# Kernel tuning notes

Measured on AMD Instinct MI355X. Metric: run time of the kernel, lower is better.

The kernel has to match this reference:

```python
import jax, jax.numpy as jnp
import numpy as np
from functools import partial

B, S, V, H, NH, NKV, M, L = 2, 2048, 51200, 1536, 24, 4, 8960, 8
DH = H // NH  # 64
EPS = 1e-6


def setup_inputs() -> dict:
    key = jax.random.key(0)
    ks = jax.random.split(key, 16)
    sc = 0.02
    w = lambda k, shape: jax.random.normal(k, shape, jnp.float32) * sc
    inp = {
        "input_ids": jax.random.randint(ks[0], (B, S), 0, V),
        "attention_mask": jnp.ones((B, S), jnp.float32),
        "embed": w(ks[1], (V, H)),
        "Wq": w(ks[2], (L, H, H)),          "bq": jnp.zeros((L, H), jnp.float32),
        "Wk": w(ks[3], (L, H, NKV * DH)),   "bk": jnp.zeros((L, NKV * DH), jnp.float32),
        "Wv": w(ks[4], (L, H, NKV * DH)),   "bv": jnp.zeros((L, NKV * DH), jnp.float32),
        "Wo": w(ks[5], (L, H, H)),
        "ln1": jnp.ones((L, H), jnp.float32),
        "ln2": jnp.ones((L, H), jnp.float32),
        "Wg": w(ks[6], (L, H, M)),
        "Wu": w(ks[7], (L, H, M)),
        "Wd": w(ks[8], (L, M, H)),
        "norm_w": jnp.ones((H,), jnp.float32),
        "W1": w(ks[9], (H, H)), "b1": jnp.zeros((H,), jnp.float32),
        "W2": w(ks[10], (H, 1)), "b2": jnp.zeros((1,), jnp.float32),
    }
    inv_freq = 1.0 / (10000.0 ** (jnp.arange(0, DH, 2, dtype=jnp.float32) / DH))
    freqs = jnp.outer(jnp.arange(S, dtype=jnp.float32), inv_freq)  # [S, DH/2]
    emb = jnp.concatenate([freqs, freqs], axis=-1)                 # [S, DH]
    inp["cos"] = jnp.cos(emb)
    inp["sin"] = jnp.sin(emb)
    return inp


def _rms(x, w):
    var = jnp.mean(x.astype(jnp.float32) ** 2, axis=-1, keepdims=True)
    return w * (x * jax.lax.rsqrt(var + EPS)).astype(x.dtype)


def _rotate_half(x):
    x1, x2 = jnp.split(x, 2, axis=-1)
    return jnp.concatenate([-x2, x1], axis=-1)


def _forward(input_ids, attention_mask, embed, Wq, bq, Wk, bk, Wv, bv, Wo,
             ln1, ln2, Wg, Wu, Wd, norm_w, W1, b1, W2, b2, cos, sin):
    scale = 1.0 / np.sqrt(DH)
    b, s = input_ids.shape
    c = cos[None, :s, None, :]  # [1,S,1,DH]
    sn = sin[None, :s, None, :]
    rope = lambda t: t * c + _rotate_half(t) * sn
    mask0 = attention_mask[:, None, None, :] == 0  # [B,1,1,S]

    def block(x, p):
        wq, bq_, wk, bk_, wv, bv_, wo, ln1w, ln2w, wg, wu, wd = p
        h = _rms(x, ln1w)
        q = (h @ wq + bq_).reshape(b, s, NH, DH)
        k = (h @ wk + bk_).reshape(b, s, NKV, DH)
        v = (h @ wv + bv_).reshape(b, s, NKV, DH)
        q, k = rope(q), rope(k)
        k = jnp.repeat(k, NH // NKV, axis=2)  # GQA expand to NH heads
        v = jnp.repeat(v, NH // NKV, axis=2)
        scores = jnp.einsum('bqhd,bkhd->bhqk', q, k) * scale
        scores = jnp.where(mask0, -1e10, scores)
        probs = jax.nn.softmax(scores, axis=-1)  # dropout: eval mode (identity)
        attn = jnp.einsum('bhqk,bkhd->bqhd', probs, v).reshape(b, s, H)
        x = x + attn @ wo
        h = _rms(x, ln2w)
        x = x + (jax.nn.sigmoid(h @ wg) * (h @ wu)) @ wd
        return x, None

    x = embed[input_ids]  # [B,S,H]
    x, _ = jax.lax.scan(block, x, (Wq, bq, Wk, bk, Wv, bv, Wo, ln1, ln2, Wg, Wu, Wd))
    x = _rms(x, norm_w)
    h = jax.nn.gelu(x @ W1 + b1, approximate=False)  # torch nn.GELU default = exact
    return h @ W2 + b2  # [B,S,1]


def reference(input_ids, attention_mask, embed, Wq, bq, Wk, bk, Wv, bv, Wo,
              ln1, ln2, Wg, Wu, Wd, norm_w, W1, b1, W2, b2, cos, sin):
    return _forward(input_ids, attention_mask, embed, Wq, bq, Wk, bk, Wv, bv, Wo,
                    ln1, ln2, Wg, Wu, Wd, norm_w, W1, b1, W2, b2, cos, sin)
```

## Files before the change

### kernel.cpp

```cpp
#include <hip/hip_runtime.h>

typedef float f32x4 __attribute__((ext_vector_type(4)));
typedef short s16x8 __attribute__((ext_vector_type(8)));
typedef unsigned short u16;
typedef unsigned short u16x4 __attribute__((ext_vector_type(4)));
typedef unsigned short u16x8 __attribute__((ext_vector_type(8)));
typedef unsigned int u32x2 __attribute__((ext_vector_type(2)));

__device__ __forceinline__ float bf2f(u16 u){ union{unsigned int i; float f;} v; v.i=((unsigned int)u)<<16; return v.f; }
__device__ __forceinline__ u16 f2bf(float f){ union{float f; unsigned int i;} v; v.f=f; return (u16)((v.i + 0x7FFFu + ((v.i>>16)&1u))>>16); }
__device__ __forceinline__ float aexp2(float x){ float r; asm("v_exp_f32 %0, %1" : "=v"(r) : "v"(x)); return r; }
__device__ __forceinline__ unsigned int cvtpk(float lo, float hi){ unsigned int r; asm("v_cvt_pk_bf16_f32 %0, %1, %2" : "=v"(r) : "v"(lo), "v"(hi)); return r; }

#define LOG2E 1.44269504089f

__device__ __forceinline__ void gld16(const void* gp, void* lp){
  __builtin_amdgcn_global_load_lds((__attribute__((address_space(1))) void*)(void*)gp,
                                   (__attribute__((address_space(3))) void*)lp, 16, 0, 0);
}

__global__ __launch_bounds__(256) void k_embed(const int* __restrict__ ids, const float* __restrict__ emb, float* __restrict__ x){
  int r = blockIdx.x;
  int id = ids[r];
  const f32x4* src = (const f32x4*)(emb + (size_t)id*1536);
  f32x4* dst = (f32x4*)(x + (size_t)r*1536);
  for (int i = threadIdx.x; i < 384; i += 256) dst[i] = src[i];
}

__global__ __launch_bounds__(256) void k_rms(const float* __restrict__ x, const float* __restrict__ w, u16* __restrict__ h){
  int r = blockIdx.x, tid = threadIdx.x;
  const f32x4* xr = (const f32x4*)(x + (size_t)r*1536);
  f32x4 v0 = xr[tid];
  float ss = v0.x*v0.x + v0.y*v0.y + v0.z*v0.z + v0.w*v0.w;
  f32x4 v1 = {0,0,0,0};
  if (tid < 128){ v1 = xr[256+tid]; ss += v1.x*v1.x + v1.y*v1.y + v1.z*v1.z + v1.w*v1.w; }
  #pragma unroll
  for (int off=32; off; off>>=1) ss += __shfl_xor(ss, off, 64);
  __shared__ float red[4];
  if ((tid&63)==0) red[tid>>6] = ss;
  __syncthreads();
  float tot = red[0]+red[1]+red[2]+red[3];
  float invr = rsqrtf(tot*(1.f/1536.f) + 1e-6f);
  const f32x4* w4 = (const f32x4*)w;
  u16x4* h4 = (u16x4*)(h + (size_t)r*1536);
  {
    f32x4 wv = w4[tid];
    u16x4 o; o.x=f2bf(v0.x*invr*wv.x); o.y=f2bf(v0.y*invr*wv.y); o.z=f2bf(v0.z*invr*wv.z); o.w=f2bf(v0.w*invr*wv.w);
    h4[tid] = o;
  }
  if (tid < 128){
    f32x4 wv = w4[256+tid];
    u16x4 o; o.x=f2bf(v1.x*invr*wv.x); o.y=f2bf(v1.y*invr*wv.y); o.z=f2bf(v1.z*invr*wv.z); o.w=f2bf(v1.w*invr*wv.w);
    h4[256+tid] = o;
  }
}

__global__ __launch_bounds__(256) void k_rms_add(float* __restrict__ x, const float* __restrict__ P, const float* __restrict__ w, u16* __restrict__ h){
  int r = blockIdx.x, tid = threadIdx.x;
  f32x4* xr = (f32x4*)(x + (size_t)r*1536);
  const f32x4* pr = (const f32x4*)(P + (size_t)r*1536);
  f32x4 v0 = xr[tid], p0 = pr[tid];
  v0.x+=p0.x; v0.y+=p0.y; v0.z+=p0.z; v0.w+=p0.w;
  xr[tid] = v0;
  float ss = v0.x*v0.x + v0.y*v0.y + v0.z*v0.z + v0.w*v0.w;
  f32x4 v1 = {0,0,0,0};
  if (tid < 128){
    v1 = xr[256+tid]; f32x4 p1 = pr[256+tid];
    v1.x+=p1.x; v1.y+=p1.y; v1.z+=p1.z; v1.w+=p1.w;
    xr[256+tid] = v1;
    ss += v1.x*v1.x + v1.y*v1.y + v1.z*v1.z + v1.w*v1.w;
  }
  #pragma unroll
  for (int off=32; off; off>>=1) ss += __shfl_xor(ss, off, 64);
  __shared__ float red[4];
  if ((tid&63)==0) red[tid>>6] = ss;
  __syncthreads();
  float tot = red[0]+red[1]+red[2]+red[3];
  float invr = rsqrtf(tot*(1.f/1536.f) + 1e-6f);
  const f32x4* w4 = (const f32x4*)w;
  u16x4* h4 = (u16x4*)(h + (size_t)r*1536);
  {
    f32x4 wv = w4[tid];
    u16x4 o; o.x=f2bf(v0.x*invr*wv.x); o.y=f2bf(v0.y*invr*wv.y); o.z=f2bf(v0.z*invr*wv.z); o.w=f2bf(v0.w*invr*wv.w);
    h4[tid] = o;
  }
  if (tid < 128){
    f32x4 wv = w4[256+tid];
    u16x4 o; o.x=f2bf(v1.x*invr*wv.x); o.y=f2bf(v1.y*invr*wv.y); o.z=f2bf(v1.z*invr*wv.z); o.w=f2bf(v1.w*invr*wv.w);
    h4[256+tid] = o;
  }
}

__device__ __forceinline__ void cvt_tile(const float* src, int K, int N, u16* dst, int k0, int n0, int roff, int mode){
  __shared__ float T[64*72];
  int tid = threadIdx.x;
  #pragma unroll
  for (int j=0;j<4;++j){
    int i = tid + j*256;
    int row = i>>4, nf = i&15;
    f32x4 vv = *(const f32x4*)(src + (size_t)(k0+row)*N + n0 + nf*4);
    *(f32x4*)&T[row*72 + nf*4] = vv;
  }
  __syncthreads();
  #pragma unroll
  for (int j=0;j<2;++j){
    int i = tid + j*256;
    int n = i>>3, kc = i&7;
    u16x8 o;
    #pragma unroll
    for (int m=0;m<8;++m) o[m] = f2bf(T[(kc*8+m)*72 + n]);
    int gn = n0 + n;
    int dr = (mode==0) ? (roff + gn) : (((gn>>4)<<5) + ((mode==2)?16:0) + (gn&15));
    *(u16x8*)(dst + (size_t)dr*K + k0 + kc*8) = o;
  }
}

__global__ __launch_bounds__(256) void k_cvt_layer(
  const float* __restrict__ Wq, const float* __restrict__ Wk, const float* __restrict__ Wv,
  const float* __restrict__ Wo, const float* __restrict__ Wg, const float* __restrict__ Wu,
  const float* __restrict__ Wd, u16* qkvt, u16* wot, u16* gut, u16* wdt)
{
  const float* src; int K, N; u16* dst; int roff=0, mode=0;
  switch (blockIdx.y){
    case 0: src=Wq; K=1536; N=1536; dst=qkvt; break;
    case 1: src=Wk; K=1536; N=256;  dst=qkvt; roff=1536; break;
    case 2: src=Wv; K=1536; N=256;  dst=qkvt; roff=1792; break;
    case 3: src=Wo; K=1536; N=1536; dst=wot;  break;
    case 4: src=Wg; K=1536; N=8960; dst=gut;  mode=1; break;
    case 5: src=Wu; K=1536; N=8960; dst=gut;  mode=2; break;
    default: src=Wd; K=8960; N=1536; dst=wdt; break;
  }
  int ntn = N>>6;
  int nt = (K>>6)*ntn;
  int t = blockIdx.x;
  if (t >= nt) return;
  cvt_tile(src, K, N, dst, (t/ntn)<<6, (t%ntn)<<6, roff, mode);
}

__global__ __launch_bounds__(256) void k_cvt_one(const float* __restrict__ src, u16* __restrict__ dst){
  int t = blockIdx.x;
  cvt_tile(src, 1536, 1536, dst, (t/24)<<6, (t%24)<<6, 0, 0);
}

#define MODE_QKV 0
#define MODE_WO 1
#define MODE_GATEUP 2
#define MODE_DOWN 3
#define MODE_W1 4

template<int MODE>
__global__ __launch_bounds__(256) void k_gemm(
  const u16* __restrict__ A, const u16* __restrict__ Bt, int K,
  int jobsPerXcd, int nc, int ksplit, int klen,
  const float* __restrict__ bq_, const float* __restrict__ bk_, const float* __restrict__ bv_,
  float* __restrict__ xio, float* __restrict__ Pf,
  const float* __restrict__ cosT, const float* __restrict__ sinT,
  u16* __restrict__ o0, u16* __restrict__ o1, u16* __restrict__ o2)
{
  int bid = blockIdx.x;
  int xcd = bid & 7, j = bid >> 3;
  int job = xcd*jobsPerXcd + (j >> 5);
  if (job >= nc*ksplit) return;
  int rowb = j & 31;
  int col = job / ksplit;
  int ks  = job - col*ksplit;
  int kbase = ks*klen;
  int nt = klen >> 5;

  __shared__ __align__(16) u16 As[4][4096], Bs[4][4096];
  int tid = threadIdx.x;
  int lane = tid & 63, w = tid >> 6;
  int wr = w >> 1, wc = w & 1;
  int row0 = rowb * 128, col0 = col * 128;
  int l15 = lane & 15, l4 = lane >> 4;
  f32x4 acc[4][4] = {};
  const u16* aBase = A + (size_t)row0*K;
  const u16* bBase = Bt + (size_t)col0*K;
  int rr0 = tid & 127, kb0 = tid >> 7;
  int kb1 = kb0 + 2;

  auto stage = [&](int bf, int kt){
    gld16(aBase + (size_t)rr0*K + kt + kb0*8, &As[bf][tid*8]);
    gld16(bBase + (size_t)rr0*K + kt + kb0*8, &Bs[bf][tid*8]);
    gld16(aBase + (size_t)rr0*K + kt + kb1*8, &As[bf][(256+tid)*8]);
    gld16(bBase + (size_t)rr0*K + kt + kb1*8, &Bs[bf][(256+tid)*8]);
  };
  stage(0, kbase); stage(1, kbase+32); stage(2, kbase+64);

  for (int t = 0; t < nt; ++t){
    if (t < nt-2)       asm volatile("s_waitcnt vmcnt(8)" ::: "memory");
    else if (t == nt-2) asm volatile("s_waitcnt vmcnt(4)" ::: "memory");
    else                asm volatile("s_waitcnt vmcnt(0)" ::: "memory");
    __builtin_amdgcn_s_barrier();
    __builtin_amdgcn_sched_barrier(0);
    if (t+3 < nt) stage((t+3)&3, kbase + (t+3)*32);
    const u16* Ab = As[t&3];
    const u16* Bb = Bs[t&3];
    s16x8 af[4], bf_[4];
    #pragma unroll
    for (int i=0;i<4;++i) af[i]  = *(const s16x8*)&Ab[((l4<<7) + wr*64 + i*16 + l15)*8];
    #pragma unroll
    for (int jj=0;jj<4;++jj) bf_[jj] = *(const s16x8*)&Bb[((l4<<7) + wc*64 + jj*16 + l15)*8];
    __builtin_amdgcn_s_setprio(1);
    #pragma unroll
    for (int i=0;i<4;++i)
      #pragma unroll
      for (int jj=0;jj<4;++jj)
        acc[i][jj] = __builtin_amdgcn_mfma_f32_16x16x32_bf16(af[i], bf_[jj], acc[i][jj], 0, 0, 0);
    __builtin_amdgcn_s_setprio(0);
  }

  #pragma unroll
  for (int i=0;i<4;++i)
    #pragma unroll
    for (int jj=0;jj<4;++jj)
      #pragma unroll
      for (int r=0;r<4;++r){
        int row = row0 + wr*64 + i*16 + l4*4 + r;
        int c   = col0 + wc*64 + jj*16 + l15;
        float v = acc[i][jj][r];
        if constexpr (MODE == MODE_QKV){
          int b = row >> 11, s = row & 2047;
          if (c < 1536){
            int d = c & 63, hd = c >> 6;
            float vv = v + bq_[c];
            float pv = acc[i][jj^2][r] + bq_[c^32];
            float cv = cosT[s*64+d], sv = sinT[s*64+d];
            float sgn = (d<32) ? -1.f : 1.f;
            float o = (vv*cv + sgn*pv*sv)*(0.125f*LOG2E);
            o0[(size_t)(b*24+hd)*131072 + (size_t)(s>>6)*4096
               + (s&63)*64 + (((d>>3)^(s&7))<<3) + (d&7)] = f2bf(o);
          } else if (c < 1792){
            int c2 = c - 1536, d = c2 & 63, kv = c2 >> 6;
            float vv = v + bk_[c2];
            float pv = acc[i][jj^2][r] + bk_[c2^32];
            float cv = cosT[s*64+d], sv = sinT[s*64+d];
            float sgn = (d<32) ? -1.f : 1.f;
            float o = vv*cv + sgn*pv*sv;
            o1[(size_t)(b*4+kv)*131072 + (size_t)(s>>6)*4096
               + (s&63)*64 + (((d>>3)^(s&7))<<3) + (d&7)] = f2bf(o);
          } else {
            int c2 = c - 1792, d = c2 & 63, kv = c2 >> 6;
            float vv = v + bv_[c2];
            o2[(size_t)(b*4+kv)*131072 + (size_t)(s>>6)*4096
               + d*64 + ((((s>>3)&7)^(d&7))<<3) + (s&7)] = f2bf(vv);
          }
        } else if constexpr (MODE == MODE_WO){
          xio[(size_t)row*1536 + c] += v;
        } else if constexpr (MODE == MODE_W1){
          v += bq_[c];
          float ge = 0.5f * v * (1.f + erff(v * 0.70710678118f));
          o0[(size_t)row*1536 + c] = f2bf(ge);
        }
      }
}

template<int MODE>
__global__ __launch_bounds__(512,2) void k_gemm256(
  const u16* __restrict__ A, const u16* __restrict__ Bt, int K,
  int nrt, int ksplit, int klen,
  float* __restrict__ xio, float* __restrict__ Pf, u16* __restrict__ o0)
{
  int bid = blockIdx.x;
  int wgid = (bid & 7)*(gridDim.x >> 3) + (bid >> 3);
  int nj = nrt*ksplit;
  int ct = wgid / nj; int r2 = wgid - ct*nj;
  int rt = r2 / ksplit; int ks = r2 - rt*ksplit;

  __shared__ __align__(16) u16 lds[2][2][16384];
  int tid = threadIdx.x;
  int lane = tid & 63, wid = tid >> 6;
  int wm = wid >> 2, wn = wid & 3;
  int l15 = lane & 15, l4 = lane >> 4;
  int lsw = l15 & 7;
  int row0 = rt*256, col0 = ct*256;
  int kbase = ks*klen*64;

  const u16* aB = A  + (size_t)row0*K + kbase;
  const u16* bB = Bt + (size_t)col0*K + kbase;
  int rsub = tid >> 3;
  int gsw  = (lane & 7) ^ ((lane >> 3) & 7);

  f32x4 acc[8][4] = {};

  auto sgA = [&](int bf, int kt, int c){
    gld16(aB + (size_t)(c*64 + rsub)*K + kt*64 + gsw*8, &lds[bf][0][(c*512+tid)*8]);
  };
  auto sgB = [&](int bf, int kt, int c){
    gld16(bB + (size_t)(c*64 + rsub)*K + kt*64 + gsw*8, &lds[bf][1][(c*512+tid)*8]);
  };

  sgB(0,0,0); sgB(0,0,1); sgB(0,0,2); sgB(0,0,3);
  sgA(0,0,0); sgA(0,0,2); sgA(0,0,1); sgA(0,0,3);

  for (int t = 0; t < klen; ++t){
    int b = t & 1, nb = b ^ 1;
    bool hasNext = (t+1 < klen);
    const u16* Ab = lds[b][0];
    const u16* Bb = lds[b][1];

    asm volatile("s_waitcnt vmcnt(2)" ::: "memory");
    __builtin_amdgcn_s_barrier();
    __builtin_amdgcn_sched_barrier(0);
    if (hasNext){ sgB(nb, t+1, 0); sgB(nb, t+1, 1); }

    s16x8 bf_[4][2];
    #pragma unroll
    for (int j=0;j<4;++j)
      #pragma unroll
      for (int ksu=0;ksu<2;++ksu)
        bf_[j][ksu] = *(const s16x8*)&Bb[(wn*64 + j*16 + l15)*64 + (((ksu*4+l4)^lsw)<<3)];

    {
      s16x8 af[2][2];
      #pragma unroll
      for (int ii=0;ii<2;++ii)
        #pragma unroll
        for (int ksu=0;ksu<2;++ksu)
          af[ii][ksu] = *(const s16x8*)&Ab[(wm*128 + ii*16 + l15)*64 + (((ksu*4+l4)^lsw)<<3)];
      __builtin_amdgcn_s_setprio(1);
      #pragma unroll
      for (int ii=0;ii<2;++ii)
        #pragma unroll
        for (int j=0;j<4;++j)
          #pragma unroll
          for (int ksu=0;ksu<2;++ksu)
            acc[ii][j] = __builtin_amdgcn_mfma_f32_16x16x32_bf16(af[ii][ksu], bf_[j][ksu], acc[ii][j], 0,0,0);
      __builtin_amdgcn_s_setprio(0);
    }
    if (hasNext){ sgB(nb, t+1, 2); sgB(nb, t+1, 3); }
    {
      s16x8 af[2][2];
      #pragma unroll
      for (int ii=0;ii<2;++ii)
        #pragma unroll
        for (int ksu=0;ksu<2;++ksu)
          af[ii][ksu] = *(const s16x8*)&Ab[(wm*128 + 32 + ii*16 + l15)*64 + (((ksu*4+l4)^lsw)<<3)];
      __builtin_amdgcn_s_setprio(1);
      #pragma unroll
      for (int ii=0;ii<2;++ii)
        #pragma unroll
        for (int j=0;j<4;++j)
          #pragma unroll
          for (int ksu=0;ksu<2;++ksu)
            acc[2+ii][j] = __builtin_amdgcn_mfma_f32_16x16x32_bf16(af[ii][ksu], bf_[j][ksu], acc[2+ii][j], 0,0,0);
      __builtin_amdgcn_s_setprio(0);
    }

    if (hasNext) asm volatile("s_waitcnt vmcnt(4)" ::: "memory");
    else         asm volatile("s_waitcnt vmcnt(0)" ::: "memory");
    __builtin_amdgcn_s_barrier();
    __builtin_amdgcn_sched_barrier(0);
    if (hasNext){ sgA(nb, t+1, 0); sgA(nb, t+1, 2); }

    {
      s16x8 af[2][2];
      #pragma unroll
      for (int ii=0;ii<2;++ii)
        #pragma unroll
        for (int ksu=0;ksu<2;++ksu)
          af[ii][ksu] = *(const s16x8*)&Ab[(wm*128 + 64 + ii*16 + l15)*64 + (((ksu*4+l4)^lsw)<<3)];
      __builtin_amdgcn_s_setprio(1);
      #pragma unroll
      for (int ii=0;ii<2;++ii)
        #pragma unroll
        for (int j=0;j<4;++j)
          #pragma unroll
          for (int ksu=0;ksu<2;++ksu)
            acc[4+ii][j] = __builtin_amdgcn_mfma_f32_16x16x32_bf16(af[ii][ksu], bf_[j][ksu], acc[4+ii][j], 0,0,0);
      __builtin_amdgcn_s_setprio(0);
    }
    if (hasNext){ sgA(nb, t+1, 1); sgA(nb, t+1, 3); }
    {
      s16x8 af[2][2];
      #pragma unroll
      for (int ii=0;ii<2;++ii)
        #pragma unroll
        for (int ksu=0;ksu<2;++ksu)
          af[ii][ksu] = *(const s16x8*)&Ab[(wm*128 + 96 + ii*16 + l15)*64 + (((ksu*4+l4)^lsw)<<3)];
      __builtin_amdgcn_s_setprio(1);
      #pragma unroll
      for (int ii=0;ii<2;++ii)
        #pragma unroll
        for (int j=0;j<4;++j)
          #pragma unroll
          for (int ksu=0;ksu<2;++ksu)
            acc[6+ii][j] = __builtin_amdgcn_mfma_f32_16x16x32_bf16(af[ii][ksu], bf_[j][ksu], acc[6+ii][j], 0,0,0);
      __builtin_amdgcn_s_setprio(0);
    }
  }

  if constexpr (MODE == MODE_GATEUP){
    #pragma unroll
    for (int i=0;i<8;++i)
      #pragma unroll
      for (int j2=0;j2<4;j2+=2)
        #pragma unroll
        for (int r=0;r<4;++r){
          int row = row0 + wm*128 + i*16 + l4*4 + r;
          int cp  = col0 + wn*64 + j2*16 + l15;
          float gv = acc[i][j2][r], uv = acc[i][j2+1][r];
          float sg = 1.f/(1.f + __expf(-gv));
          int n = ((cp>>5)<<4) + (cp&15);
          o0[(size_t)row*8960 + n] = f2bf(sg*uv);
        }
  } else {
    #pragma unroll
    for (int i=0;i<8;++i)
      #pragma unroll
      for (int j=0;j<4;++j)
        #pragma unroll
        for (int r=0;r<4;++r){
          int row = row0 + wm*128 + i*16 + l4*4 + r;
          int c   = col0 + wn*64 + j*16 + l15;
          float v = acc[i][j][r];
          if (ks == 0) Pf[(size_t)row*1536 + c] = v;
          else         xio[(size_t)row*1536 + c] += v;
        }
  }
}

__global__ __launch_bounds__(256) void k_attn(
  const u16* __restrict__ q, const u16* __restrict__ k, const u16* __restrict__ v,
  const float* __restrict__ mask, u16* __restrict__ attn)
{
  __shared__ __align__(16) u16 Qs[4096];
  __shared__ __align__(16) u16 Kd[2][4096];
  __shared__ __align__(16) u16 Vd[2][4096];
  __shared__ u16 Msh[2048];
  int tid = threadIdx.x;
  int lane = tid & 63, w = tid >> 6;
  int qb = blockIdx.x;
  int bh = blockIdx.y;
  int b = bh / 24, hh = bh % 24, kv = hh / 6;
  int l15 = lane & 15, l4 = lane >> 4;
  int sw = l15 & 7;

  const u16* qhead = q + ((size_t)(b*24 + hh))*131072 + qb*4096;
  const u16* khead = k + ((size_t)(b*4  + kv))*131072;
  const u16* vhead = v + ((size_t)(b*4  + kv))*131072;

  {
    const f32x4* m4 = (const f32x4*)(mask + b*2048);
    const u16 mvis = f2bf(-4.f*LOG2E);
    const u16 mmask = f2bf(-1.4e9f);
    for (int i = tid; i < 512; i += 256){
      f32x4 mv = m4[i];
      u16x4 o;
      o.x = (mv.x==0.f) ? mmask : mvis;
      o.y = (mv.y==0.f) ? mmask : mvis;
      o.z = (mv.z==0.f) ? mmask : mvis;
      o.w = (mv.w==0.f) ? mmask : mvis;
      *(u16x4*)&Msh[i*4] = o;
    }
  }
  gld16(qhead + tid*8,       &Qs[tid*8]);
  gld16(qhead + (256+tid)*8, &Qs[(256+tid)*8]);

  auto stage = [&](int bf, int kt){
    gld16(khead + kt*4096 + tid*8,       &Kd[bf][tid*8]);
    gld16(khead + kt*4096 + (256+tid)*8, &Kd[bf][(256+tid)*8]);
    gld16(vhead + kt*4096 + tid*8,       &Vd[bf][tid*8]);
    gld16(vhead + kt*4096 + (256+tid)*8, &Vd[bf][(256+tid)*8]);
  };
  stage(0, 0);

  s16x8 aq0, aq1;
  f32x4 oacc[4] = {};
  float lsum = 0.f;
  u16* Pw = &Qs[w*1024];

  for (int t = 0; t < 32; ++t){
    asm volatile("s_waitcnt vmcnt(0)" ::: "memory");
    __builtin_amdgcn_s_barrier();
    __builtin_amdgcn_sched_barrier(0);
    if (t == 0){
      int qrow = w*16 + l15;
      aq0 = *(const s16x8*)&Qs[qrow*64 + (( l4    ^ sw)<<3)];
      aq1 = *(const s16x8*)&Qs[qrow*64 + (((4+l4) ^ sw)<<3)];
    }
    if (t+1 < 32) stage((t+1)&1, t+1);
    const u16* Kb = Kd[t&1];
    const u16* Vb = Vd[t&1];
    f32x4 sk[4] = {};
    __builtin_amdgcn_s_setprio(1);
    #pragma unroll
    for (int kn=0; kn<4; ++kn){
      int krow = kn*16 + l15;
      s16x8 a0 = *(const s16x8*)&Kb[krow*64 + (( l4    ^ sw)<<3)];
      s16x8 a1 = *(const s16x8*)&Kb[krow*64 + (((4+l4) ^ sw)<<3)];
      sk[kn] = __builtin_amdgcn_mfma_f32_16x16x32_bf16(a0, aq0, sk[kn], 0,0,0);
      sk[kn] = __builtin_amdgcn_mfma_f32_16x16x32_bf16(a1, aq1, sk[kn], 0,0,0);
    }
    __builtin_amdgcn_s_setprio(0);
    #pragma unroll
    for (int kn=0; kn<4; ++kn){
      u16x4 mv = *(const u16x4*)&Msh[t*64 + kn*16 + l4*4];
      float p0 = aexp2(sk[kn][0] + bf2f(mv.x));
      float p1 = aexp2(sk[kn][1] + bf2f(mv.y));
      float p2 = aexp2(sk[kn][2] + bf2f(mv.z));
      float p3 = aexp2(sk[kn][3] + bf2f(mv.w));
      lsum += (p0 + p1) + (p2 + p3);
      u32x2 pk; pk.x = cvtpk(p0, p1); pk.y = cvtpk(p2, p3);
      int g = kn*2 + (l4>>1);
      *(u32x2*)&Pw[l15*64 + ((g ^ sw)<<3) + (l4&1)*4] = pk;
    }
    __builtin_amdgcn_s_setprio(1);
    #pragma unroll
    for (int ksu=0; ksu<2; ++ksu){
      s16x8 ap = *(const s16x8*)&Pw[l15*64 + (((ksu*4+l4) ^ sw)<<3)];
      #pragma unroll
      for (int dg=0; dg<4; ++dg){
        s16x8 bv = *(const s16x8*)&Vb[(dg*16+l15)*64 + (((ksu*4+l4) ^ sw)<<3)];
        oacc[dg] = __builtin_amdgcn_mfma_f32_16x16x32_bf16(ap, bv, oacc[dg], 0,0,0);
      }
    }
    __builtin_amdgcn_s_setprio(0);
  }
  lsum += __shfl_xor(lsum, 16, 64);
  lsum += __shfl_xor(lsum, 32, 64);
  float invq[4];
  #pragma unroll
  for (int r=0;r<4;++r) invq[r] = 1.f / __shfl(lsum, l4*4 + r, 64);
  #pragma unroll
  for (int dg=0;dg<4;++dg)
    #pragma unroll
    for (int r=0;r<4;++r){
      int token = b*2048 + qb*64 + w*16 + l4*4 + r;
      int col = hh*64 + dg*16 + l15;
      attn[(size_t)token*1536 + col] = f2bf(oacc[dg][r] * invq[r]);
    }
}

__global__ __launch_bounds__(256) void k_gemv(const u16* __restrict__ h2, const float* __restrict__ W2, const float* __restrict__ b2, float* __restrict__ out){
  int tid = threadIdx.x, lane = tid & 63, w = tid >> 6;
  int r = blockIdx.x*4 + w;
  const u16* hr = h2 + (size_t)r*1536;
  float s = 0.f;
  #pragma unroll
  for (int i=0;i<24;++i){ int c = lane + i*64; s += bf2f(hr[c]) * W2[c]; }
  #pragma unroll
  for (int off=32; off; off>>=1) s += __shfl_xor(s, off, 64);
  if (lane == 0) out[r] = s + b2[0];
}

extern "C" void kernel_launch(void* const* d_in, const int* in_sizes, int n_in,
                              void* d_out, int out_size, void* d_ws, size_t ws_size,
                              hipStream_t stream)
{
  const int*   ids   = (const int*)d_in[0];
  const float* mask  = (const float*)d_in[1];
  const float* embed = (const float*)d_in[2];
  const float* Wq    = (const float*)d_in[3];
  const float* bq    = (const float*)d_in[4];
  const float* Wk    = (const float*)d_in[5];
  const float* bk    = (const float*)d_in[6];
  const float* Wv    = (const float*)d_in[7];
  const float* bv    = (const float*)d_in[8];
  const float* Wo    = (const float*)d_in[9];
  const float* ln1   = (const float*)d_in[10];
  const float* ln2   = (const float*)d_in[11];
  const float* Wg    = (const float*)d_in[12];
  const float* Wu    = (const float*)d_in[13];
  const float* Wd    = (const float*)d_in[14];
  const float* nw    = (const float*)d_in[15];
  const float* W1    = (const float*)d_in[16];
  const float* b1    = (const float*)d_in[17];
  const float* W2    = (const float*)d_in[18];
  const float* b2    = (const float*)d_in[19];
  const float* cosT  = (const float*)d_in[20];
  const float* sinT  = (const float*)d_in[21];

  char* ws = (char*)d_ws;
  float* x   = (float*)(ws + 0);
  u16* h     = (u16*)(ws + 25165824);
  u16* qb_   = (u16*)(ws + 37748736);
  u16* kb_   = (u16*)(ws + 50331648);
  u16* vb_   = (u16*)(ws + 52428800);
  u16* attn  = (u16*)(ws + 54525952);
  u16* g     = (u16*)(ws + 67108864);
  u16* qkvt  = (u16*)(ws + 140509184);
  u16* wot   = (u16*)(ws + 146800640);
  u16* gut   = (u16*)(ws + 151519232);
  u16* wdt   = (u16*)(ws + 206569472);
  float* Pf  = (float*)(ws + 37748736);
  (void)in_sizes; (void)n_in; (void)out_size; (void)ws_size;

  k_embed<<<4096, 256, 0, stream>>>(ids, embed, x);
  for (int l = 0; l < 8; ++l){
    k_cvt_layer<<<dim3(3360,7), 256, 0, stream>>>(
      Wq + (size_t)l*1536*1536, Wk + (size_t)l*1536*256, Wv + (size_t)l*1536*256,
      Wo + (size_t)l*1536*1536, Wg + (size_t)l*1536*8960, Wu + (size_t)l*1536*8960,
      Wd + (size_t)l*8960*1536, qkvt, wot, gut, wdt);
    if (l == 0) k_rms<<<4096, 256, 0, stream>>>(x, ln1, h);
    else        k_rms_add<<<4096, 256, 0, stream>>>(x, Pf, ln1 + l*1536, h);
    k_gemm<MODE_QKV><<<512, 256, 0, stream>>>(h, qkvt, 1536, 2, 16, 1, 1536,
        bq + l*1536, bk + l*256, bv + l*256, nullptr, nullptr, cosT, sinT, qb_, kb_, vb_);
    k_attn<<<dim3(32,48), 256, 0, stream>>>(qb_, kb_, vb_, mask, attn);
    k_gemm<MODE_WO><<<512, 256, 0, stream>>>(attn, wot, 1536, 2, 12, 1, 1536,
        nullptr, nullptr, nullptr, x, nullptr, nullptr, nullptr, nullptr, nullptr, nullptr);
    k_rms<<<4096, 256, 0, stream>>>(x, ln2 + l*1536, h);
    k_gemm256<MODE_GATEUP><<<1120, 512, 0, stream>>>(h, gut, 1536, 16, 1, 24,
        nullptr, nullptr, g);
    k_gemm256<MODE_DOWN><<<192, 512, 0, stream>>>(g, wdt, 8960, 16, 2, 70,
        x, Pf, nullptr);
  }
  k_cvt_one<<<576, 256, 0, stream>>>(W1, wot);
  k_rms_add<<<4096, 256, 0, stream>>>(x, Pf, nw, h);
  k_gemm<MODE_W1><<<512, 256, 0, stream>>>(h, wot, 1536, 2, 12, 1, 1536,
      b1, nullptr, nullptr, nullptr, nullptr, nullptr, nullptr, attn, nullptr, nullptr);
  k_gemv<<<1024, 256, 0, stream>>>(attn, W2, b2, (float*)d_out);
}
```

Measured before the change: 5.425 ms.

## Use supertile job mapping for GEMMs and precompute attention mask table

Replaces the per-kernel block-to-tile mappings with a shared XCD-aware supertile mapping (SR x SC groups of tiles), so blocks on the same XCD work on neighbouring row/column tiles and reuse A/B panels in L2. Grid sizes for WO and W1 shrink to exactly match the tile count, removing idle early-exit blocks. The attention mask is converted once into a bf16 table by a new kernel, and attention reads it from global memory instead of rebuilding it in LDS in every block. This adds global loads in the inner softmax loop in exchange for less LDS use and less setup per block.

```diff
diff --git a/kernel.cpp b/kernel.cpp
--- a/kernel.cpp
+++ b/kernel.cpp
@@ -19,12 +19,32 @@
                                    (__attribute__((address_space(3))) void*)lp, 16, 0, 0);
 }
 
+__device__ __forceinline__ void job_map(int bid, int gridx, int nrt, int nct, int ksplit,
+                                        int SR, int SC, int& rt, int& ct, int& ks){
+  int jpx = gridx >> 3;
+  int wgid = (bid & 7)*jpx + (bid >> 3);
+  int nj1 = nrt*nct;
+  ks = wgid / nj1; int rr = wgid - ks*nj1;
+  int spc = SR*SC, nstc = nct/SC;
+  int st = rr / spc, win = rr - st*spc;
+  int str_ = st / nstc, stc = st - str_*nstc;
+  int wr = win / SC, wc = win - wr*SC;
+  rt = str_*SR + wr;
+  ct = stc*SC + wc;
+}
+
 __global__ __launch_bounds__(256) void k_embed(const int* __restrict__ ids, const float* __restrict__ emb, float* __restrict__ x){
   int r = blockIdx.x;
   int id = ids[r];
   const f32x4* src = (const f32x4*)(emb + (size_t)id*1536);
   f32x4* dst = (f32x4*)(x + (size_t)r*1536);
   for (int i = threadIdx.x; i < 384; i += 256) dst[i] = src[i];
+}
+
+__global__ __launch_bounds__(256) void k_mask(const float* __restrict__ mask, u16* __restrict__ mtab){
+  int i = blockIdx.x*256 + threadIdx.x;
+  float mv = mask[i];
+  mtab[i] = (mv==0.f) ? f2bf(-1.4e9f) : f2bf(-4.f*LOG2E);
 }
 
 __global__ __launch_bounds__(256) void k_rms(const float* __restrict__ x, const float* __restrict__ w, u16* __restrict__ h){
@@ -151,19 +171,14 @@
 template<int MODE>
 __global__ __launch_bounds__(256) void k_gemm(
   const u16* __restrict__ A, const u16* __restrict__ Bt, int K,
-  int jobsPerXcd, int nc, int ksplit, int klen,
+  int nrt, int nct, int ksplit, int klen, int SR, int SC,
   const float* __restrict__ bq_, const float* __restrict__ bk_, const float* __restrict__ bv_,
   float* __restrict__ xio, float* __restrict__ Pf,
   const float* __restrict__ cosT, const float* __restrict__ sinT,
   u16* __restrict__ o0, u16* __restrict__ o1, u16* __restrict__ o2)
 {
-  int bid = blockIdx.x;
-  int xcd = bid & 7, j = bid >> 3;
-  int job = xcd*jobsPerXcd + (j >> 5);
-  if (job >= nc*ksplit) return;
-  int rowb = j & 31;
-  int col = job / ksplit;
-  int ks  = job - col*ksplit;
+  int rt, ct, ks;
+  job_map(blockIdx.x, gridDim.x, nrt, nct, ksplit, SR, SC, rt, ct, ks);
   int kbase = ks*klen;
   int nt = klen >> 5;
 
@@ -171,7 +186,7 @@
   int tid = threadIdx.x;
   int lane = tid & 63, w = tid >> 6;
   int wr = w >> 1, wc = w & 1;
-  int row0 = rowb * 128, col0 = col * 128;
+  int row0 = rt * 128, col0 = ct * 128;
   int l15 = lane & 15, l4 = lane >> 4;
   f32x4 acc[4][4] = {};
   const u16* aBase = A + (size_t)row0*K;
@@ -258,14 +273,11 @@
 template<int MODE>
 __global__ __launch_bounds__(512,2) void k_gemm256(
   const u16* __restrict__ A, const u16* __restrict__ Bt, int K,
-  int nrt, int ksplit, int klen,
+  int nrt, int nct, int ksplit, int klen, int SR, int SC,
   float* __restrict__ xio, float* __restrict__ Pf, u16* __restrict__ o0)
 {
-  int bid = blockIdx.x;
-  int wgid = (bid & 7)*(gridDim.x >> 3) + (bid >> 3);
-  int nj = nrt*ksplit;
-  int ct = wgid / nj; int r2 = wgid - ct*nj;
-  int rt = r2 / ksplit; int ks = r2 - rt*ksplit;
+  int rt, ct, ks;
+  job_map(blockIdx.x, gridDim.x, nrt, nct, ksplit, SR, SC, rt, ct, ks);
 
   __shared__ __align__(16) u16 lds[2][2][16384];
   int tid = threadIdx.x;
@@ -422,12 +434,11 @@
 
 __global__ __launch_bounds__(256) void k_attn(
   const u16* __restrict__ q, const u16* __restrict__ k, const u16* __restrict__ v,
-  const float* __restrict__ mask, u16* __restrict__ attn)
+  const u16* __restrict__ mtab, u16* __restrict__ attn)
 {
   __shared__ __align__(16) u16 Qs[4096];
   __shared__ __align__(16) u16 Kd[2][4096];
   __shared__ __align__(16) u16 Vd[2][4096];
-  __shared__ u16 Msh[2048];
   int tid = threadIdx.x;
   int lane = tid & 63, w = tid >> 6;
   int qb = blockIdx.x;
@@ -439,21 +450,8 @@
   const u16* qhead = q + ((size_t)(b*24 + hh))*131072 + qb*4096;
   const u16* khead = k + ((size_t)(b*4  + kv))*131072;
   const u16* vhead = v + ((size_t)(b*4  + kv))*131072;
-
-  {
-    const f32x4* m4 = (const f32x4*)(mask + b*2048);
-    const u16 mvis = f2bf(-4.f*LOG2E);
-    const u16 mmask = f2bf(-1.4e9f);
-    for (int i = tid; i < 512; i += 256){
-      f32x4 mv = m4[i];
-      u16x4 o;
-      o.x = (mv.x==0.f) ? mmask : mvis;
-      o.y = (mv.y==0.f) ? mmask : mvis;
-      o.z = (mv.z==0.f) ? mmask : mvis;
-      o.w = (mv.w==0.f) ? mmask : mvis;
-      *(u16x4*)&Msh[i*4] = o;
-    }
-  }
+  const u16* mrow = mtab + b*2048;
+
   gld16(qhead + tid*8,       &Qs[tid*8]);
   gld16(qhead + (256+tid)*8, &Qs[(256+tid)*8]);
 
@@ -495,7 +493,7 @@
     __builtin_amdgcn_s_setprio(0);
     #pragma unroll
     for (int kn=0; kn<4; ++kn){
-      u16x4 mv = *(const u16x4*)&Msh[t*64 + kn*16 + l4*4];
+      u16x4 mv = *(const u16x4*)&mrow[t*64 + kn*16 + l4*4];
       float p0 = aexp2(sk[kn][0] + bf2f(mv.x));
       float p1 = aexp2(sk[kn][1] + bf2f(mv.y));
       float p2 = aexp2(sk[kn][2] + bf2f(mv.z));
@@ -583,10 +581,12 @@
   u16* wot   = (u16*)(ws + 146800640);
   u16* gut   = (u16*)(ws + 151519232);
   u16* wdt   = (u16*)(ws + 206569472);
+  u16* mtab  = (u16*)(ws + 234094592);
   float* Pf  = (float*)(ws + 37748736);
   (void)in_sizes; (void)n_in; (void)out_size; (void)ws_size;
 
   k_embed<<<4096, 256, 0, stream>>>(ids, embed, x);
+  k_mask<<<16, 256, 0, stream>>>(mask, mtab);
   for (int l = 0; l < 8; ++l){
     k_cvt_layer<<<dim3(3360,7), 256, 0, stream>>>(
       Wq + (size_t)l*1536*1536, Wk + (size_t)l*1536*256, Wv + (size_t)l*1536*256,
@@ -594,20 +594,20 @@
       Wd + (size_t)l*8960*1536, qkvt, wot, gut, wdt);
     if (l == 0) k_rms<<<4096, 256, 0, stream>>>(x, ln1, h);
     else        k_rms_add<<<4096, 256, 0, stream>>>(x, Pf, ln1 + l*1536, h);
-    k_gemm<MODE_QKV><<<512, 256, 0, stream>>>(h, qkvt, 1536, 2, 16, 1, 1536,
+    k_gemm<MODE_QKV><<<512, 256, 0, stream>>>(h, qkvt, 1536, 32, 16, 1, 1536, 8, 4,
         bq + l*1536, bk + l*256, bv + l*256, nullptr, nullptr, cosT, sinT, qb_, kb_, vb_);
-    k_attn<<<dim3(32,48), 256, 0, stream>>>(qb_, kb_, vb_, mask, attn);
-    k_gemm<MODE_WO><<<512, 256, 0, stream>>>(attn, wot, 1536, 2, 12, 1, 1536,
+    k_attn<<<dim3(32,48), 256, 0, stream>>>(qb_, kb_, vb_, mtab, attn);
+    k_gemm<MODE_WO><<<384, 256, 0, stream>>>(attn, wot, 1536, 32, 12, 1, 1536, 8, 4,
         nullptr, nullptr, nullptr, x, nullptr, nullptr, nullptr, nullptr, nullptr, nullptr);
     k_rms<<<4096, 256, 0, stream>>>(x, ln2 + l*1536, h);
-    k_gemm256<MODE_GATEUP><<<1120, 512, 0, stream>>>(h, gut, 1536, 16, 1, 24,
+    k_gemm256<MODE_GATEUP><<<1120, 512, 0, stream>>>(h, gut, 1536, 16, 70, 1, 24, 8, 10,
         nullptr, nullptr, g);
-    k_gemm256<MODE_DOWN><<<192, 512, 0, stream>>>(g, wdt, 8960, 16, 2, 70,
+    k_gemm256<MODE_DOWN><<<192, 512, 0, stream>>>(g, wdt, 8960, 16, 6, 2, 70, 4, 6,
         x, Pf, nullptr);
   }
   k_cvt_one<<<576, 256, 0, stream>>>(W1, wot);
   k_rms_add<<<4096, 256, 0, stream>>>(x, Pf, nw, h);
-  k_gemm<MODE_W1><<<512, 256, 0, stream>>>(h, wot, 1536, 2, 12, 1, 1536,
+  k_gemm<MODE_W1><<<384, 256, 0, stream>>>(h, wot, 1536, 32, 12, 1, 1536, 8, 4,
       b1, nullptr, nullptr, nullptr, nullptr, nullptr, nullptr, attn, nullptr, nullptr);
   k_gemv<<<1024, 256, 0, stream>>>(attn, W2, b2, (float*)d_out);
 }
```

Result: no change. 5.340 ms (-1.6%).
